# Kernel optimization log

Hardware: AMD Instinct MI355X
Metric: run time of the kernel (lower is better)

The kernel has to match this reference:

```python
import jax, jax.numpy as jnp
import numpy as np

N_NODES = 50000
N_EDGES = 800000
D_FEAT = 64
UNITS = 128  # concat=True -> each kernel maps D_FEAT -> UNITS//2


def setup_inputs() -> dict:
    key = jax.random.key(0)
    k1, k2, k3, k4, k5 = jax.random.split(key, 5)
    x = jax.random.normal(k1, (N_NODES, D_FEAT), dtype=jnp.float32)
    edge_index = jax.random.randint(k2, (2, N_EDGES), 0, N_NODES, dtype=jnp.int64)
    edge_weight = jax.random.uniform(k3, (N_EDGES,), dtype=jnp.float32)
    glorot = np.sqrt(6.0 / (D_FEAT + UNITS // 2)).astype(np.float32)
    self_kernel = jax.random.uniform(k4, (D_FEAT, UNITS // 2), dtype=jnp.float32, minval=-glorot, maxval=glorot)
    neighbor_kernel = jax.random.uniform(k5, (D_FEAT, UNITS // 2), dtype=jnp.float32, minval=-glorot, maxval=glorot)
    bias = jnp.zeros((UNITS,), dtype=jnp.float32)
    return {"x": x, "edge_index": edge_index, "edge_weight": edge_weight,
            "self_kernel": self_kernel, "neighbor_kernel": neighbor_kernel, "bias": bias}


def reference(x, edge_index, edge_weight, self_kernel, neighbor_kernel, bias):
    num_nodes = x.shape[0]
    row, col = edge_index[0], edge_index[1]  # row: target node, col: source neighbor
    # gather neighbor features and apply edge weights
    neighbor_x = x[col] * edge_weight[:, None]  # [E, D]
    # segment-mean over incoming edges of each target node
    sums = jax.ops.segment_sum(neighbor_x, row, num_segments=num_nodes)  # [N, D]
    counts = jax.ops.segment_sum(jnp.ones_like(edge_weight), row, num_segments=num_nodes)  # [N]
    neighbor_mean = sums / jnp.maximum(counts, 1.0)[:, None]
    # dual projection + concat (concat=True)
    from_self = x @ self_kernel              # [N, UNITS//2]
    from_neigh = neighbor_mean @ neighbor_kernel  # [N, UNITS//2]
    h = jnp.concatenate([from_self, from_neigh], axis=1) + bias
    h = jax.nn.relu(h)
    # normalize=False -> no l2 normalize
    return h
```

## Files before the change

kernel.cpp:

```cpp
#include <hip/hip_runtime.h>


typedef unsigned long long ull;
typedef __attribute__((ext_vector_type(8))) short bf16x8;
typedef __attribute__((ext_vector_type(4))) float f32x4;

constexpr int N_NODES = 50000;
constexpr int N_EDGES = 800000;
constexpr int D = 64;
constexpr int UNITS = 128;
constexpr int NB = (N_NODES + 255) / 256;
constexpr int SC_EPT = 16;
constexpr int SC_THREADS = 256;
constexpr int SC_CHUNK = SC_EPT * SC_THREADS;
constexpr int SC_BLOCKS = (N_EDGES + SC_CHUNK - 1) / SC_CHUNK;
constexpr int NS_EPT = 24;
constexpr int PREP_BLOCKS = 2048;
constexpr int AP_BLOCKS = N_NODES / 16;

__device__ __forceinline__ unsigned f2bf(float f) {
    unsigned u = __float_as_uint(f);
    return (u + 0x7fffu + ((u >> 16) & 1u)) >> 16;
}
__device__ __forceinline__ float bf2f(unsigned b) {
    return __uint_as_float(b << 16);
}

__global__ __launch_bounds__(256) void prep(const float* __restrict__ x,
                                            unsigned* __restrict__ xh,
                                            const int* __restrict__ ei,
                                            int* __restrict__ partial) {
    constexpr int XW = N_NODES * (D / 2);
    for (int i = blockIdx.x * 256 + threadIdx.x; i < XW; i += PREP_BLOCKS * 256) {
        const float2 v = ((const float2*)x)[i];
        xh[i] = f2bf(v.x) | (f2bf(v.y) << 16);
    }
    if (blockIdx.x < SC_BLOCKS) {
        __shared__ int lh[NB];
        for (int i = threadIdx.x; i < NB; i += 256) lh[i] = 0;
        __syncthreads();
        const int base4 = blockIdx.x * (SC_CHUNK / 4);
        #pragma unroll
        for (int j = 0; j < 4; ++j) {
            const int idx4 = base4 + threadIdx.x + j * 256;
            if (idx4 * 4 < N_EDGES) {
                const int4 r4 = ((const int4*)ei)[idx4];
                atomicAdd(&lh[r4.x >> 8], 1);
                atomicAdd(&lh[r4.y >> 8], 1);
                atomicAdd(&lh[r4.z >> 8], 1);
                atomicAdd(&lh[r4.w >> 8], 1);
            }
        }
        __syncthreads();
        int* row = partial + (size_t)blockIdx.x * NB;
        for (int i = threadIdx.x; i < NB; i += 256) row[i] = lh[i];
    }
}

__global__ __launch_bounds__(256) void scan_cols(int* __restrict__ partial,
                                                 int* __restrict__ btot) {
    __shared__ int s[256];
    const int b = blockIdx.x;
    const int t = threadIdx.x;
    const int v = (t < SC_BLOCKS) ? partial[(size_t)t * NB + b] : 0;
    s[t] = v;
    __syncthreads();
    for (int d2 = 1; d2 < 256; d2 <<= 1) {
        int u = (t >= d2) ? s[t - d2] : 0;
        __syncthreads();
        s[t] += u;
        __syncthreads();
    }
    if (t < SC_BLOCKS) partial[(size_t)t * NB + b] = s[t] - v;
    if (t == 255) btot[b] = s[255];
}

__global__ __launch_bounds__(SC_THREADS) void edge_scatter(const int* __restrict__ ei,
                                                           const float* __restrict__ ew,
                                                           const int* __restrict__ partial,
                                                           const int* __restrict__ btot,
                                                           ull* __restrict__ packed) {
    __shared__ int sb[256];
    __shared__ int lbase[NB];
    __shared__ int lcur[NB];
    const int t = threadIdx.x;
    const int bv = (t < NB) ? btot[t] : 0;
    sb[t] = bv;
    __syncthreads();
    for (int d2 = 1; d2 < 256; d2 <<= 1) {
        int u = (t >= d2) ? sb[t - d2] : 0;
        __syncthreads();
        sb[t] += u;
        __syncthreads();
    }
    const int* row = partial + (size_t)blockIdx.x * NB;
    if (t < NB) {
        lbase[t] = (sb[t] - bv) + row[t];
        lcur[t]  = 0;
    }
    __syncthreads();

    const int base4 = blockIdx.x * (SC_CHUNK / 4);
    int4   r4[4];
    int4   c4[4];
    float4 w4[4];
    #pragma unroll
    for (int j = 0; j < 4; ++j) {
        const int idx4 = base4 + t + j * 256;
        if (idx4 * 4 < N_EDGES) {
            r4[j] = ((const int4*)ei)[idx4];
            c4[j] = ((const int4*)(ei + N_EDGES))[idx4];
            w4[j] = ((const float4*)ew)[idx4];
        } else {
            r4[j] = make_int4(-1, -1, -1, -1);
            c4[j] = make_int4(0, 0, 0, 0);
            w4[j] = make_float4(0.f, 0.f, 0.f, 0.f);
        }
    }
    #pragma unroll
    for (int j = 0; j < 4; ++j) {
        const int   rr[4] = {r4[j].x, r4[j].y, r4[j].z, r4[j].w};
        const int   cc[4] = {c4[j].x, c4[j].y, c4[j].z, c4[j].w};
        const float ww[4] = {w4[j].x, w4[j].y, w4[j].z, w4[j].w};
        #pragma unroll
        for (int k = 0; k < 4; ++k) {
            const int r = rr[k];
            if (r >= 0) {
                const int bb   = r >> 8;
                const int lpos = atomicAdd(&lcur[bb], 1);
                const unsigned hi = (unsigned)cc[k] | ((unsigned)(r & 255) << 16);
                packed[lbase[bb] + lpos] = ((ull)hi << 32) | (ull)(unsigned)__float_as_uint(ww[k]);
            }
        }
    }
}

__global__ __launch_bounds__(256) void node_sort(const int* __restrict__ btot,
                                                 int* __restrict__ offs,
                                                 const ull* __restrict__ packed,
                                                 unsigned* __restrict__ cedges) {
    __shared__ int cur[256];
    __shared__ int sc[256];
    __shared__ int sBase, sEnd;
    const int b = blockIdx.x;
    const int t = threadIdx.x;

    const int bv = (t < NB) ? btot[t] : 0;
    sc[t] = bv;
    __syncthreads();
    for (int d2 = 1; d2 < 256; d2 <<= 1) {
        int u = (t >= d2) ? sc[t - d2] : 0;
        __syncthreads();
        sc[t] += u;
        __syncthreads();
    }
    if (t == b) { sBase = sc[t] - bv; sEnd = sc[t]; }
    __syncthreads();
    const int s = sBase;
    const int e = sEnd;

    ull st[NS_EPT];
    #pragma unroll
    for (int i = 0; i < NS_EPT; ++i) {
        const int idx = s + t + i * 256;
        st[i] = (idx < e) ? packed[idx] : ~0ull;
    }
    cur[t] = 0;
    __syncthreads();
    #pragma unroll
    for (int i = 0; i < NS_EPT; ++i) {
        if (st[i] != ~0ull) atomicAdd(&cur[(int)((st[i] >> 48) & 0xff)], 1);
    }
    __syncthreads();
    const int v = cur[t];
    sc[t] = v;
    __syncthreads();
    for (int d2 = 1; d2 < 256; d2 <<= 1) {
        int u = (t >= d2) ? sc[t - d2] : 0;
        __syncthreads();
        sc[t] += u;
        __syncthreads();
    }
    const int excl = sc[t] - v;
    const int n = b * 256 + t;
    if (n < N_NODES) offs[n] = s + excl;
    if (b == 0 && t == 0) offs[N_NODES] = N_EDGES;
    cur[t] = excl;
    __syncthreads();
    #pragma unroll
    for (int i = 0; i < NS_EPT; ++i) {
        if (st[i] != ~0ull) {
            const int r8  = (int)((st[i] >> 48) & 0xff);
            const int pos = atomicAdd(&cur[r8], 1);
            const unsigned hi  = (unsigned)(st[i] >> 32);
            const unsigned col = hi & 0xffffu;
            const unsigned wbf = f2bf(__uint_as_float((unsigned)st[i]));
            cedges[s + pos] = (col << 16) | wbf;
        }
    }
}

__global__ __launch_bounds__(512) void sage_agg_proj(const unsigned* __restrict__ xh,
                                                     const int* __restrict__ offs,
                                                     const unsigned* __restrict__ cedges,
                                                     const float* __restrict__ skern,
                                                     const float* __restrict__ nkern,
                                                     const float* __restrict__ bias,
                                                     float* __restrict__ out) {
    __shared__ unsigned meanl[16][36];
    const int tid = threadIdx.x;
    const int n0  = blockIdx.x * 16;

    {
        const int hw  = tid >> 5;
        const int l32 = tid & 31;
        const int eg  = l32 >> 3;
        const int wq  = l32 & 7;
        const int n = n0 + hw;
        const int s = offs[n];
        const int t = offs[n + 1];

        float ax0 = 0.f, ay0 = 0.f, ax1 = 0.f, ay1 = 0.f;
        float ax2 = 0.f, ay2 = 0.f, ax3 = 0.f, ay3 = 0.f;
        float bx0 = 0.f, by0 = 0.f, bx1 = 0.f, by1 = 0.f;
        float bx2 = 0.f, by2 = 0.f, bx3 = 0.f, by3 = 0.f;

        if (t > s) {
            const int tm1 = t - 1;
            for (int g = s; g < t; g += 8) {
                const int eA = g + eg;
                const int eB = g + 4 + eg;
                const unsigned cA = cedges[min(eA, tm1)];
                const unsigned cB = cedges[min(eB, tm1)];
                const float wA = (eA < t) ? bf2f(cA & 0xffffu) : 0.0f;
                const float wB = (eB < t) ? bf2f(cB & 0xffffu) : 0.0f;
                const uint4 vA = *(const uint4*)(xh + (size_t)(cA >> 16) * (D / 2) + wq * 4);
                const uint4 vB = *(const uint4*)(xh + (size_t)(cB >> 16) * (D / 2) + wq * 4);
                ax0 = fmaf(__uint_as_float(vA.x << 16),         wA, ax0);
                ay0 = fmaf(__uint_as_float(vA.x & 0xffff0000u), wA, ay0);
                ax1 = fmaf(__uint_as_float(vA.y << 16),         wA, ax1);
                ay1 = fmaf(__uint_as_float(vA.y & 0xffff0000u), wA, ay1);
                ax2 = fmaf(__uint_as_float(vA.z << 16),         wA, ax2);
                ay2 = fmaf(__uint_as_float(vA.z & 0xffff0000u), wA, ay2);
                ax3 = fmaf(__uint_as_float(vA.w << 16),         wA, ax3);
                ay3 = fmaf(__uint_as_float(vA.w & 0xffff0000u), wA, ay3);
                bx0 = fmaf(__uint_as_float(vB.x << 16),         wB, bx0);
                by0 = fmaf(__uint_as_float(vB.x & 0xffff0000u), wB, by0);
                bx1 = fmaf(__uint_as_float(vB.y << 16),         wB, bx1);
                by1 = fmaf(__uint_as_float(vB.y & 0xffff0000u), wB, by1);
                bx2 = fmaf(__uint_as_float(vB.z << 16),         wB, bx2);
                by2 = fmaf(__uint_as_float(vB.z & 0xffff0000u), wB, by2);
                bx3 = fmaf(__uint_as_float(vB.w << 16),         wB, bx3);
                by3 = fmaf(__uint_as_float(vB.w & 0xffff0000u), wB, by3);
            }
        }
        float sx0 = ax0 + bx0, sy0 = ay0 + by0;
        float sx1 = ax1 + bx1, sy1 = ay1 + by1;
        float sx2 = ax2 + bx2, sy2 = ay2 + by2;
        float sx3 = ax3 + bx3, sy3 = ay3 + by3;
        sx0 += __shfl_xor(sx0, 8);  sx0 += __shfl_xor(sx0, 16);
        sy0 += __shfl_xor(sy0, 8);  sy0 += __shfl_xor(sy0, 16);
        sx1 += __shfl_xor(sx1, 8);  sx1 += __shfl_xor(sx1, 16);
        sy1 += __shfl_xor(sy1, 8);  sy1 += __shfl_xor(sy1, 16);
        sx2 += __shfl_xor(sx2, 8);  sx2 += __shfl_xor(sx2, 16);
        sy2 += __shfl_xor(sy2, 8);  sy2 += __shfl_xor(sy2, 16);
        sx3 += __shfl_xor(sx3, 8);  sx3 += __shfl_xor(sx3, 16);
        sy3 += __shfl_xor(sy3, 8);  sy3 += __shfl_xor(sy3, 16);

        if (eg == 0) {
            const float inv = 1.0f / fmaxf((float)(t - s), 1.0f);
            uint4 r;
            r.x = f2bf(sx0 * inv) | (f2bf(sy0 * inv) << 16);
            r.y = f2bf(sx1 * inv) | (f2bf(sy1 * inv) << 16);
            r.z = f2bf(sx2 * inv) | (f2bf(sy2 * inv) << 16);
            r.w = f2bf(sx3 * inv) | (f2bf(sy3 * inv) << 16);
            *(uint4*)&meanl[hw][wq * 4] = r;
        }
    }
    __syncthreads();

    {
        const int w    = tid >> 6;
        const int lane = tid & 63;
        const int r16  = lane & 15;
        const int g    = lane >> 4;
        const float* K = (w < 4) ? skern : nkern;
        const int col  = (w & 3) * 16 + r16;

        bf16x8 b0, b1;
        #pragma unroll
        for (int j = 0; j < 8; ++j) {
            b0[j] = (short)f2bf(K[(8 * g + j) * 64 + col]);
            b1[j] = (short)f2bf(K[(32 + 8 * g + j) * 64 + col]);
        }

        bf16x8 a0, a1;
        if (w < 4) {
            const unsigned* xrow = xh + (size_t)(n0 + r16) * (D / 2);
            a0 = *(const bf16x8*)(xrow + 4 * g);
            a1 = *(const bf16x8*)(xrow + 16 + 4 * g);
        } else {
            a0 = *(const bf16x8*)&meanl[r16][4 * g];
            a1 = *(const bf16x8*)&meanl[r16][16 + 4 * g];
        }

        f32x4 c = {0.f, 0.f, 0.f, 0.f};
        c = __builtin_amdgcn_mfma_f32_16x16x32_bf16(a0, b0, c, 0, 0, 0);
        c = __builtin_amdgcn_mfma_f32_16x16x32_bf16(a1, b1, c, 0, 0, 0);

        const int ocol = (w < 4 ? 0 : 64) + (w & 3) * 16 + r16;
        const float bj = bias[ocol];
        #pragma unroll
        for (int r = 0; r < 4; ++r) {
            out[(size_t)(n0 + 4 * g + r) * UNITS + ocol] = fmaxf(c[r] + bj, 0.0f);
        }
    }
}

extern "C" void kernel_launch(void* const* d_in, const int* in_sizes, int n_in,
                              void* d_out, int out_size, void* d_ws, size_t ws_size,
                              hipStream_t stream) {
    const float* x     = (const float*)d_in[0];
    const int*   ei    = (const int*)  d_in[1];
    const float* ew    = (const float*)d_in[2];
    const float* skern = (const float*)d_in[3];
    const float* nkern = (const float*)d_in[4];
    const float* bias  = (const float*)d_in[5];
    float* out = (float*)d_out;

    auto align256 = [](size_t v) { return (v + 255) & ~size_t(255); };
    const size_t szM  = align256((size_t)SC_BLOCKS * NB * sizeof(int));
    const size_t szT  = align256((size_t)NB * sizeof(int));
    const size_t szNO = align256((size_t)(N_NODES + 1) * sizeof(int));
    const size_t szP  = align256((size_t)N_EDGES * sizeof(ull));
    const size_t szC  = align256((size_t)N_EDGES * sizeof(unsigned));

    char* w = (char*)d_ws;
    int*      partial = (int*)w;
    int*      btot    = (int*)(w + szM);
    int*      offs    = (int*)(w + szM + szT);
    ull*      packed  = (ull*)(w + szM + szT + szNO);
    unsigned* cedges  = (unsigned*)(w + szM + szT + szNO + szP);
    unsigned* xh      = (unsigned*)(w + szM + szT + szNO + szP + szC);
    (void)ws_size; (void)in_sizes; (void)n_in; (void)out_size;

    prep         <<<PREP_BLOCKS, 256, 0, stream>>>(x, xh, ei, partial);
    scan_cols    <<<NB, 256, 0, stream>>>(partial, btot);
    edge_scatter <<<SC_BLOCKS, SC_THREADS, 0, stream>>>(ei, ew, partial, btot, packed);
    node_sort    <<<NB, SC_THREADS, 0, stream>>>(btot, offs, packed, cedges);
    sage_agg_proj<<<AP_BLOCKS, 512, 0, stream>>>(xh, offs, cedges, skern, nkern, bias, out);
}
```

Baseline: 60.44 us.

## Fuse CSR build kernels into one persistent kernel with grid barriers

Merges scan_cols, edge_scatter and node_sort into a single kernel launched with NB (196) blocks, separated by atomic-counter grid barriers, and zeroes the barrier counters in prep. This removes two kernel launches and their inter-kernel gaps, and precomputes block offsets once per block. It relies on all 196 blocks being co-resident on the device; otherwise it deadlocks. The edge_scatter and node_sort phases each happen to use 196 blocks (SC_BLOCKS equals NB), so the mapping stays consistent.

```diff
diff --git a/kernel.cpp b/kernel.cpp
--- a/kernel.cpp
+++ b/kernel.cpp
@@ -26,10 +26,25 @@
     return __uint_as_float(b << 16);
 }
 
+__device__ __forceinline__ void gridbar(int* ctr, int target) {
+    __threadfence();
+    __syncthreads();
+    if (threadIdx.x == 0) {
+        __hip_atomic_fetch_add(ctr, 1, __ATOMIC_RELEASE, __HIP_MEMORY_SCOPE_AGENT);
+        while (__hip_atomic_load(ctr, __ATOMIC_ACQUIRE, __HIP_MEMORY_SCOPE_AGENT) < target) {
+            __builtin_amdgcn_s_sleep(8);
+        }
+    }
+    __syncthreads();
+    __threadfence();
+}
+
 __global__ __launch_bounds__(256) void prep(const float* __restrict__ x,
                                             unsigned* __restrict__ xh,
                                             const int* __restrict__ ei,
-                                            int* __restrict__ partial) {
+                                            int* __restrict__ partial,
+                                            int* __restrict__ bar) {
+    if (blockIdx.x == 0 && threadIdx.x < 8) bar[threadIdx.x] = 0;
     constexpr int XW = N_NODES * (D / 2);
     for (int i = blockIdx.x * 256 + threadIdx.x; i < XW; i += PREP_BLOCKS * 256) {
         const float2 v = ((const float2*)x)[i];
@@ -57,145 +72,135 @@
     }
 }
 
-__global__ __launch_bounds__(256) void scan_cols(int* __restrict__ partial,
-                                                 int* __restrict__ btot) {
-    __shared__ int s[256];
+__global__ __launch_bounds__(256) void csr_fused(const int* __restrict__ ei,
+                                                 const float* __restrict__ ew,
+                                                 int* __restrict__ partial,
+                                                 int* __restrict__ btot,
+                                                 int* __restrict__ bar,
+                                                 int* __restrict__ offs,
+                                                 ull* __restrict__ packed,
+                                                 unsigned* __restrict__ cedges) {
+    __shared__ int lcur[NB];
+    __shared__ int lbase[NB];
+    __shared__ int sb[256];
+    __shared__ int bofs[NB + 1];
     const int b = blockIdx.x;
     const int t = threadIdx.x;
-    const int v = (t < SC_BLOCKS) ? partial[(size_t)t * NB + b] : 0;
-    s[t] = v;
+
+    {
+        const int v = (t < SC_BLOCKS) ? partial[(size_t)t * NB + b] : 0;
+        sb[t] = v;
+        __syncthreads();
+        for (int d2 = 1; d2 < 256; d2 <<= 1) {
+            int u = (t >= d2) ? sb[t - d2] : 0;
+            __syncthreads();
+            sb[t] += u;
+            __syncthreads();
+        }
+        if (t < SC_BLOCKS) partial[(size_t)t * NB + b] = sb[t] - v;
+        if (t == 255) btot[b] = sb[255];
+    }
+    gridbar(bar + 0, NB);
+
+    {
+        const int bv = (t < NB) ? btot[t] : 0;
+        sb[t] = bv;
+        __syncthreads();
+        for (int d2 = 1; d2 < 256; d2 <<= 1) {
+            int u = (t >= d2) ? sb[t - d2] : 0;
+            __syncthreads();
+            sb[t] += u;
+            __syncthreads();
+        }
+        if (t < NB) bofs[t] = sb[t] - bv;
+        if (t == 255) bofs[NB] = sb[255];
+        __syncthreads();
+        for (int i = t; i < NB; i += 256) {
+            lbase[i] = bofs[i] + partial[(size_t)b * NB + i];
+            lcur[i]  = 0;
+        }
+    }
     __syncthreads();
-    for (int d2 = 1; d2 < 256; d2 <<= 1) {
-        int u = (t >= d2) ? s[t - d2] : 0;
-        __syncthreads();
-        s[t] += u;
-        __syncthreads();
-    }
-    if (t < SC_BLOCKS) partial[(size_t)t * NB + b] = s[t] - v;
-    if (t == 255) btot[b] = s[255];
-}
-
-__global__ __launch_bounds__(SC_THREADS) void edge_scatter(const int* __restrict__ ei,
-                                                           const float* __restrict__ ew,
-                                                           const int* __restrict__ partial,
-                                                           const int* __restrict__ btot,
-                                                           ull* __restrict__ packed) {
-    __shared__ int sb[256];
-    __shared__ int lbase[NB];
-    __shared__ int lcur[NB];
-    const int t = threadIdx.x;
-    const int bv = (t < NB) ? btot[t] : 0;
-    sb[t] = bv;
-    __syncthreads();
-    for (int d2 = 1; d2 < 256; d2 <<= 1) {
-        int u = (t >= d2) ? sb[t - d2] : 0;
-        __syncthreads();
-        sb[t] += u;
-        __syncthreads();
-    }
-    const int* row = partial + (size_t)blockIdx.x * NB;
-    if (t < NB) {
-        lbase[t] = (sb[t] - bv) + row[t];
-        lcur[t]  = 0;
-    }
-    __syncthreads();
-
-    const int base4 = blockIdx.x * (SC_CHUNK / 4);
-    int4   r4[4];
-    int4   c4[4];
-    float4 w4[4];
-    #pragma unroll
-    for (int j = 0; j < 4; ++j) {
-        const int idx4 = base4 + t + j * 256;
-        if (idx4 * 4 < N_EDGES) {
-            r4[j] = ((const int4*)ei)[idx4];
-            c4[j] = ((const int4*)(ei + N_EDGES))[idx4];
-            w4[j] = ((const float4*)ew)[idx4];
-        } else {
-            r4[j] = make_int4(-1, -1, -1, -1);
-            c4[j] = make_int4(0, 0, 0, 0);
-            w4[j] = make_float4(0.f, 0.f, 0.f, 0.f);
-        }
-    }
-    #pragma unroll
-    for (int j = 0; j < 4; ++j) {
-        const int   rr[4] = {r4[j].x, r4[j].y, r4[j].z, r4[j].w};
-        const int   cc[4] = {c4[j].x, c4[j].y, c4[j].z, c4[j].w};
-        const float ww[4] = {w4[j].x, w4[j].y, w4[j].z, w4[j].w};
-        #pragma unroll
-        for (int k = 0; k < 4; ++k) {
-            const int r = rr[k];
-            if (r >= 0) {
-                const int bb   = r >> 8;
-                const int lpos = atomicAdd(&lcur[bb], 1);
-                const unsigned hi = (unsigned)cc[k] | ((unsigned)(r & 255) << 16);
-                packed[lbase[bb] + lpos] = ((ull)hi << 32) | (ull)(unsigned)__float_as_uint(ww[k]);
-            }
-        }
-    }
-}
-
-__global__ __launch_bounds__(256) void node_sort(const int* __restrict__ btot,
-                                                 int* __restrict__ offs,
-                                                 const ull* __restrict__ packed,
-                                                 unsigned* __restrict__ cedges) {
-    __shared__ int cur[256];
-    __shared__ int sc[256];
-    __shared__ int sBase, sEnd;
-    const int b = blockIdx.x;
-    const int t = threadIdx.x;
-
-    const int bv = (t < NB) ? btot[t] : 0;
-    sc[t] = bv;
-    __syncthreads();
-    for (int d2 = 1; d2 < 256; d2 <<= 1) {
-        int u = (t >= d2) ? sc[t - d2] : 0;
-        __syncthreads();
-        sc[t] += u;
-        __syncthreads();
-    }
-    if (t == b) { sBase = sc[t] - bv; sEnd = sc[t]; }
-    __syncthreads();
-    const int s = sBase;
-    const int e = sEnd;
-
-    ull st[NS_EPT];
-    #pragma unroll
-    for (int i = 0; i < NS_EPT; ++i) {
-        const int idx = s + t + i * 256;
-        st[i] = (idx < e) ? packed[idx] : ~0ull;
-    }
-    cur[t] = 0;
-    __syncthreads();
-    #pragma unroll
-    for (int i = 0; i < NS_EPT; ++i) {
-        if (st[i] != ~0ull) atomicAdd(&cur[(int)((st[i] >> 48) & 0xff)], 1);
-    }
-    __syncthreads();
-    const int v = cur[t];
-    sc[t] = v;
-    __syncthreads();
-    for (int d2 = 1; d2 < 256; d2 <<= 1) {
-        int u = (t >= d2) ? sc[t - d2] : 0;
-        __syncthreads();
-        sc[t] += u;
-        __syncthreads();
-    }
-    const int excl = sc[t] - v;
-    const int n = b * 256 + t;
-    if (n < N_NODES) offs[n] = s + excl;
-    if (b == 0 && t == 0) offs[N_NODES] = N_EDGES;
-    cur[t] = excl;
-    __syncthreads();
-    #pragma unroll
-    for (int i = 0; i < NS_EPT; ++i) {
-        if (st[i] != ~0ull) {
-            const int r8  = (int)((st[i] >> 48) & 0xff);
-            const int pos = atomicAdd(&cur[r8], 1);
-            const unsigned hi  = (unsigned)(st[i] >> 32);
-            const unsigned col = hi & 0xffffu;
-            const unsigned wbf = f2bf(__uint_as_float((unsigned)st[i]));
-            cedges[s + pos] = (col << 16) | wbf;
+
+    {
+        const int base4 = b * (SC_CHUNK / 4);
+        int4   r4[4];
+        int4   c4[4];
+        float4 w4[4];
+        #pragma unroll
+        for (int j = 0; j < 4; ++j) {
+            const int idx4 = base4 + t + j * 256;
+            if (idx4 * 4 < N_EDGES) {
+                r4[j] = ((const int4*)ei)[idx4];
+                c4[j] = ((const int4*)(ei + N_EDGES))[idx4];
+                w4[j] = ((const float4*)ew)[idx4];
+            } else {
+                r4[j] = make_int4(-1, -1, -1, -1);
+                c4[j] = make_int4(0, 0, 0, 0);
+                w4[j] = make_float4(0.f, 0.f, 0.f, 0.f);
+            }
+        }
+        #pragma unroll
+        for (int j = 0; j < 4; ++j) {
+            const int   rr[4] = {r4[j].x, r4[j].y, r4[j].z, r4[j].w};
+            const int   cc[4] = {c4[j].x, c4[j].y, c4[j].z, c4[j].w};
+            const float ww[4] = {w4[j].x, w4[j].y, w4[j].z, w4[j].w};
+            #pragma unroll
+            for (int k = 0; k < 4; ++k) {
+                const int r = rr[k];
+                if (r >= 0) {
+                    const int bb   = r >> 8;
+                    const int lpos = atomicAdd(&lcur[bb], 1);
+                    const unsigned hi = (unsigned)cc[k] | ((unsigned)(r & 255) << 16);
+                    packed[lbase[bb] + lpos] = ((ull)hi << 32) | (ull)(unsigned)__float_as_uint(ww[k]);
+                }
+            }
+        }
+    }
+    gridbar(bar + 1, NB);
+
+    {
+        const int s = bofs[b];
+        const int e = bofs[b + 1];
+        ull st[NS_EPT];
+        #pragma unroll
+        for (int i = 0; i < NS_EPT; ++i) {
+            const int idx = s + t + i * 256;
+            st[i] = (idx < e) ? packed[idx] : ~0ull;
+        }
+        lcur[t] = 0;
+        __syncthreads();
+        #pragma unroll
+        for (int i = 0; i < NS_EPT; ++i) {
+            if (st[i] != ~0ull) atomicAdd(&lcur[(int)((st[i] >> 48) & 0xff)], 1);
+        }
+        __syncthreads();
+        const int v = lcur[t];
+        sb[t] = v;
+        __syncthreads();
+        for (int d2 = 1; d2 < 256; d2 <<= 1) {
+            int u = (t >= d2) ? sb[t - d2] : 0;
+            __syncthreads();
+            sb[t] += u;
+            __syncthreads();
+        }
+        const int excl = sb[t] - v;
+        const int n = b * 256 + t;
+        if (n < N_NODES) offs[n] = s + excl;
+        if (b == 0 && t == 0) offs[N_NODES] = N_EDGES;
+        __syncthreads();
+        lcur[t] = excl;
+        __syncthreads();
+        #pragma unroll
+        for (int i = 0; i < NS_EPT; ++i) {
+            if (st[i] != ~0ull) {
+                const int r8  = (int)((st[i] >> 48) & 0xff);
+                const int pos = atomicAdd(&lcur[r8], 1);
+                const unsigned hi  = (unsigned)(st[i] >> 32);
+                const unsigned col = hi & 0xffffu;
+                const unsigned wbf = f2bf(__uint_as_float((unsigned)st[i]));
+                cedges[s + pos] = (col << 16) | wbf;
+            }
         }
     }
 }
@@ -331,6 +336,7 @@
     auto align256 = [](size_t v) { return (v + 255) & ~size_t(255); };
     const size_t szM  = align256((size_t)SC_BLOCKS * NB * sizeof(int));
     const size_t szT  = align256((size_t)NB * sizeof(int));
+    const size_t szB  = align256(8 * sizeof(int));
     const size_t szNO = align256((size_t)(N_NODES + 1) * sizeof(int));
     const size_t szP  = align256((size_t)N_EDGES * sizeof(ull));
     const size_t szC  = align256((size_t)N_EDGES * sizeof(unsigned));
@@ -338,15 +344,14 @@
     char* w = (char*)d_ws;
     int*      partial = (int*)w;
     int*      btot    = (int*)(w + szM);
-    int*      offs    = (int*)(w + szM + szT);
-    ull*      packed  = (ull*)(w + szM + szT + szNO);
-    unsigned* cedges  = (unsigned*)(w + szM + szT + szNO + szP);
-    unsigned* xh      = (unsigned*)(w + szM + szT + szNO + szP + szC);
+    int*      bar     = (int*)(w + szM + szT);
+    int*      offs    = (int*)(w + szM + szT + szB);
+    ull*      packed  = (ull*)(w + szM + szT + szB + szNO);
+    unsigned* cedges  = (unsigned*)(w + szM + szT + szB + szNO + szP);
+    unsigned* xh      = (unsigned*)(w + szM + szT + szB + szNO + szP + szC);
     (void)ws_size; (void)in_sizes; (void)n_in; (void)out_size;
 
-    prep         <<<PREP_BLOCKS, 256, 0, stream>>>(x, xh, ei, partial);
-    scan_cols    <<<NB, 256, 0, stream>>>(partial, btot);
-    edge_scatter <<<SC_BLOCKS, SC_THREADS, 0, stream>>>(ei, ew, partial, btot, packed);
-    node_sort    <<<NB, SC_THREADS, 0, stream>>>(btot, offs, packed, cedges);
+    prep         <<<PREP_BLOCKS, 256, 0, stream>>>(x, xh, ei, partial, bar);
+    csr_fused    <<<NB, 256, 0, stream>>>(ei, ew, partial, btot, bar, offs, packed, cedges);
     sage_agg_proj<<<AP_BLOCKS, 512, 0, stream>>>(xh, offs, cedges, skern, nkern, bias, out);
 }
```

New measurement: 148.7 us. 146% more time.
